# Kernel optimization log

Hardware: AMD Instinct MI355X
Metric: run time of the kernel (lower is better)

Reference implementation:

```python
import jax, jax.numpy as jnp
import numpy as np

N, IN, HID, OUT = 8192, 512, 256, 128

def setup_inputs() -> dict:
    key = jax.random.key(0)
    k1, k2, k3, k4 = jax.random.split(key, 4)
    adj = jax.random.uniform(k1, (N, N), dtype=jnp.float32)
    feature = jax.random.normal(k2, (N, IN), dtype=jnp.float32)
    W1 = jax.random.normal(k3, (IN, HID), dtype=jnp.float32) * (1.0 / np.sqrt(IN))
    b1 = jnp.zeros((HID,), dtype=jnp.float32)
    W2 = jax.random.normal(k4, (HID, OUT), dtype=jnp.float32) * (1.0 / np.sqrt(HID))
    b2 = jnp.zeros((OUT,), dtype=jnp.float32)
    return {"adj": adj, "feature": feature, "W1": W1, "b1": b1, "W2": W2, "b2": b2}

def reference(adj, feature, W1, b1, W2, b2):
    # GCN encoder: layer1 (relu) then layer2 (linear output)
    h = jax.nn.relu(adj @ (feature @ W1) + b1)   # [N, HID]
    h = adj @ (h @ W2) + b2                      # [N, OUT]
    # InnerProductDecoder: sigmoid(flatten(h @ h.T))
    logits = h @ h.T                             # [N, N]
    h_noise = jax.nn.sigmoid(logits.reshape(-1)) # [N*N]
    return (h_noise, h)
```

## Files before the change

### kernel.cpp

```cpp
#include <hip/hip_runtime.h>


typedef __bf16 bf16x8_t __attribute__((ext_vector_type(8)));
typedef __bf16 bf16x4_t __attribute__((ext_vector_type(4)));
typedef float  f32x4_t  __attribute__((ext_vector_type(4)));

#define MFMA_BF16(a, b, c) __builtin_amdgcn_mfma_f32_16x16x32_bf16((a), (b), (c), 0, 0, 0)

__device__ __forceinline__ bf16x8_t cvt8(float4 u, float4 v) {
    bf16x8_t o;
    o[0] = (__bf16)u.x; o[1] = (__bf16)u.y; o[2] = (__bf16)u.z; o[3] = (__bf16)u.w;
    o[4] = (__bf16)v.x; o[5] = (__bf16)v.y; o[6] = (__bf16)v.z; o[7] = (__bf16)v.w;
    return o;
}

__device__ __forceinline__ void gload_lds16(const void* g, void* l) {
    __builtin_amdgcn_global_load_lds(
        (const __attribute__((address_space(1))) unsigned int*)g,
        (__attribute__((address_space(3))) unsigned int*)l, 16, 0, 0);
}

__global__ __launch_bounds__(256) void cast_adj(
    const float* __restrict__ adj, __bf16* __restrict__ ab)
{
    const size_t j = (size_t)blockIdx.x * 256 + threadIdx.x;
    const float4* p = (const float4*)adj + j * 2;
    float4 u = p[0], v = p[1];
    *(bf16x8_t*)(ab + j * 8) = cvt8(u, v);
}

__global__ __launch_bounds__(256) void cast_all(
    const float* __restrict__ feat, const float* __restrict__ W1,
    const float* __restrict__ W2, __bf16* __restrict__ fb,
    __bf16* __restrict__ w1t, __bf16* __restrict__ w2t)
{
    const int j = blockIdx.x * 256 + threadIdx.x;
    if (j < 524288) {
        const float4* p = (const float4*)feat + (size_t)j * 2;
        float4 u = p[0], v = p[1];
        *(bf16x8_t*)(fb + (size_t)j * 8) = cvt8(u, v);
    } else if (j < 524288 + 131072) {
        int t = j - 524288;
        int k = t >> 8, n = t & 255;
        w1t[n * 512 + k] = (__bf16)W1[t];
    } else if (j < 524288 + 131072 + 32768) {
        int t = j - 655360;
        int k = t >> 7, n = t & 127;
        w2t[n * 256 + k] = (__bf16)W2[t];
    }
}

template<int MT, int WC>
__global__ __launch_bounds__(256, 2) void gemm_bt_cbf16(
    const __bf16* __restrict__ X, const __bf16* __restrict__ Yb,
    __bf16* __restrict__ C, int K, int N)
{
    constexpr int WR = 4 / WC;
    constexpr int BM = WR * MT * 16;
    constexpr int BN = WC * 64;
    const int mblk = blockIdx.x, nblk = blockIdx.y;
    const int w = threadIdx.x >> 6, lane = threadIdx.x & 63;
    const int wr = w / WC, wc = w % WC;
    const int q = lane >> 4, l16 = lane & 15;
    const int mbase = mblk * BM + wr * (MT * 16);
    const int nbase = nblk * BN + wc * 64;

    f32x4_t acc[MT][4];
    const f32x4_t z = {0.f, 0.f, 0.f, 0.f};
#pragma unroll
    for (int i = 0; i < MT; i++)
#pragma unroll
        for (int jj = 0; jj < 4; jj++) acc[i][jj] = z;

    const __bf16* Xr[MT];
    const __bf16* Yr[4];
#pragma unroll
    for (int i = 0; i < MT; i++) Xr[i] = X + (size_t)(mbase + i * 16 + l16) * K + q * 8;
#pragma unroll
    for (int jj = 0; jj < 4; jj++) Yr[jj] = Yb + (size_t)(nbase + jj * 16 + l16) * K + q * 8;

    for (int k = 0; k < K; k += 32) {
        bf16x8_t a[MT], b[4];
#pragma unroll
        for (int i = 0; i < MT; i++) a[i] = *(const bf16x8_t*)(Xr[i] + k);
#pragma unroll
        for (int jj = 0; jj < 4; jj++) b[jj] = *(const bf16x8_t*)(Yr[jj] + k);
#pragma unroll
        for (int i = 0; i < MT; i++)
#pragma unroll
            for (int jj = 0; jj < 4; jj++) acc[i][jj] = MFMA_BF16(a[i], b[jj], acc[i][jj]);
    }

#pragma unroll
    for (int i = 0; i < MT; i++)
#pragma unroll
        for (int jj = 0; jj < 4; jj++) {
            const int row0 = mbase + i * 16 + q * 4;
            const int col = nbase + jj * 16 + l16;
#pragma unroll
            for (int r = 0; r < 4; r++)
                C[(size_t)(row0 + r) * N + col] = (__bf16)acc[i][jj][r];
        }
}

template<int NN>
__global__ __launch_bounds__(256, 2) void gemm_adj_m97(
    const __bf16* __restrict__ A, const __bf16* __restrict__ Y,
    float* __restrict__ P, int kchunk)
{
    __shared__ __bf16 As[2][8192];
    __shared__ __bf16 Bs[2][8192];

    const int mblk = blockIdx.x;
    const int nblk = blockIdx.y;
    const int ks   = blockIdx.z;
    const int w = threadIdx.x >> 6, lane = threadIdx.x & 63;
    const int wr = w >> 1, wc = w & 1;
    const int q = lane >> 4, l16 = lane & 15;
    const int kbase = ks * kchunk;
    const int ntiles = kchunk >> 6;

    const int srow = lane >> 3;
    const int gdst = lane & 7;
    const __bf16* gA[4];
    const __bf16* gB[4];
    int lofs[4];
#pragma unroll
    for (int j = 0; j < 4; j++) {
        const int row = (w * 4 + j) * 8 + srow;
        const int gs = gdst ^ (row & 7);
        gA[j] = A + (size_t)(mblk * 128 + row) * 8192 + kbase + gs * 8;
        gB[j] = Y + (size_t)(nblk * 128 + row) * 8192 + kbase + gs * 8;
        lofs[j] = row * 64 + gdst * 8;
    }

    f32x4_t acc[4][4];
    const f32x4_t z = {0.f, 0.f, 0.f, 0.f};
#pragma unroll
    for (int i = 0; i < 4; i++)
#pragma unroll
        for (int jj = 0; jj < 4; jj++) acc[i][jj] = z;

#pragma unroll
    for (int j = 0; j < 4; j++) {
        gload_lds16(gA[j], &As[0][0] + lofs[j]);
        gload_lds16(gB[j], &Bs[0][0] + lofs[j]);
    }

    int buf = 0;
    for (int kt = 0; kt < ntiles; kt++) {
        __syncthreads();

        if (kt + 1 < ntiles) {
            const int koff = (kt + 1) << 6;
#pragma unroll
            for (int j = 0; j < 4; j++) {
                gload_lds16(gA[j] + koff, &As[buf ^ 1][0] + lofs[j]);
                gload_lds16(gB[j] + koff, &Bs[buf ^ 1][0] + lofs[j]);
            }
        }

        const __bf16* __restrict__ LA = &As[buf][0];
        const __bf16* __restrict__ LB = &Bs[buf][0];
#pragma unroll
        for (int s = 0; s < 2; s++) {
            bf16x8_t a[4], b[4];
#pragma unroll
            for (int i = 0; i < 4; i++) {
                const int r = wr * 64 + i * 16 + l16;
                const int g = ((s * 4 + q) ^ (r & 7)) * 8;
                a[i] = *(const bf16x8_t*)(LA + r * 64 + g);
            }
#pragma unroll
            for (int jj = 0; jj < 4; jj++) {
                const int r = wc * 64 + jj * 16 + l16;
                const int g = ((s * 4 + q) ^ (r & 7)) * 8;
                b[jj] = *(const bf16x8_t*)(LB + r * 64 + g);
            }
#pragma unroll
            for (int i = 0; i < 4; i++)
#pragma unroll
                for (int jj = 0; jj < 4; jj++)
                    acc[i][jj] = MFMA_BF16(a[i], b[jj], acc[i][jj]);
        }
        buf ^= 1;
    }

#pragma unroll
    for (int i = 0; i < 4; i++)
#pragma unroll
        for (int jj = 0; jj < 4; jj++) {
            const int row0 = mblk * 128 + wr * 64 + i * 16 + q * 4;
            const int col = nblk * 128 + wc * 64 + jj * 16 + l16;
            float* pp = P + ((size_t)ks * 8192 + row0) * NN + col;
#pragma unroll
            for (int r = 0; r < 4; r++) pp[(size_t)r * NN] = acc[i][jj][r];
        }
}

__global__ __launch_bounds__(256) void epi_relu_bias(
    const float* __restrict__ P, const float* __restrict__ bias,
    __bf16* __restrict__ H)
{
    const size_t SL = (size_t)8192 * 256;
    const size_t idx = ((size_t)blockIdx.x * 256 + threadIdx.x) * 4;
    float4 s;
    s.x = s.y = s.z = s.w = 0.f;
#pragma unroll
    for (int k = 0; k < 4; k++) {
        float4 t = *(const float4*)(P + k * SL + idx);
        s.x += t.x; s.y += t.y; s.z += t.z; s.w += t.w;
    }
    const int col = (int)(idx & 255);
    float4 bb = *(const float4*)(bias + col);
    bf16x4_t o;
    o[0] = (__bf16)fmaxf(s.x + bb.x, 0.f);
    o[1] = (__bf16)fmaxf(s.y + bb.y, 0.f);
    o[2] = (__bf16)fmaxf(s.z + bb.z, 0.f);
    o[3] = (__bf16)fmaxf(s.w + bb.w, 0.f);
    *(bf16x4_t*)(H + idx) = o;
}

__global__ __launch_bounds__(256) void epi_bias_out(
    const float* __restrict__ P, const float* __restrict__ bias,
    float* __restrict__ Hout, __bf16* __restrict__ Hbf)
{
    const size_t SL = (size_t)8192 * 128;
    const size_t idx = ((size_t)blockIdx.x * 256 + threadIdx.x) * 4;
    float4 s;
    s.x = s.y = s.z = s.w = 0.f;
#pragma unroll
    for (int k = 0; k < 8; k++) {
        float4 t = *(const float4*)(P + k * SL + idx);
        s.x += t.x; s.y += t.y; s.z += t.z; s.w += t.w;
    }
    const int col = (int)(idx & 127);
    float4 bb = *(const float4*)(bias + col);
    float4 o;
    o.x = s.x + bb.x; o.y = s.y + bb.y; o.z = s.z + bb.z; o.w = s.w + bb.w;
    *(float4*)(Hout + idx) = o;
    bf16x4_t ob;
    ob[0] = (__bf16)o.x; ob[1] = (__bf16)o.y; ob[2] = (__bf16)o.z; ob[3] = (__bf16)o.w;
    *(bf16x4_t*)(Hbf + idx) = ob;
}

__global__ __launch_bounds__(256, 2) void gemm_sig(
    const __bf16* __restrict__ H, float* __restrict__ out)
{
    const int mblk = blockIdx.x, nblk = blockIdx.y;
    const int w = threadIdx.x >> 6, lane = threadIdx.x & 63;
    const int wr = w >> 1, wc = w & 1;
    const int q = lane >> 4, l16 = lane & 15;
    const int mbase = mblk * 128 + wr * 64;
    const int nbase = nblk * 128 + wc * 64;

    f32x4_t acc[4][4];
    const f32x4_t z = {0.f, 0.f, 0.f, 0.f};
#pragma unroll
    for (int i = 0; i < 4; i++)
#pragma unroll
        for (int jj = 0; jj < 4; jj++) acc[i][jj] = z;

#pragma unroll
    for (int k = 0; k < 128; k += 32) {
        bf16x8_t a[4], b[4];
#pragma unroll
        for (int i = 0; i < 4; i++)
            a[i] = *(const bf16x8_t*)(H + (size_t)(mbase + i * 16 + l16) * 128 + k + q * 8);
#pragma unroll
        for (int jj = 0; jj < 4; jj++)
            b[jj] = *(const bf16x8_t*)(H + (size_t)(nbase + jj * 16 + l16) * 128 + k + q * 8);
#pragma unroll
        for (int i = 0; i < 4; i++)
#pragma unroll
            for (int jj = 0; jj < 4; jj++) acc[i][jj] = MFMA_BF16(a[i], b[jj], acc[i][jj]);
    }

#pragma unroll
    for (int i = 0; i < 4; i++)
#pragma unroll
        for (int jj = 0; jj < 4; jj++) {
            const int row0 = mbase + i * 16 + q * 4;
            const int col = nbase + jj * 16 + l16;
#pragma unroll
            for (int r = 0; r < 4; r++) {
                float x = acc[i][jj][r];
                out[(size_t)(row0 + r) * 8192 + col] = 1.0f / (1.0f + __expf(-x));
            }
        }
}

extern "C" void kernel_launch(void* const* d_in, const int* in_sizes, int n_in,
                              void* d_out, int out_size, void* d_ws, size_t ws_size,
                              hipStream_t stream)
{
    const float* adj  = (const float*)d_in[0];
    const float* feat = (const float*)d_in[1];
    const float* W1   = (const float*)d_in[2];
    const float* b1   = (const float*)d_in[3];
    const float* W2   = (const float*)d_in[4];
    const float* b2   = (const float*)d_in[5];
    float* out = (float*)d_out;

    char* p = (char*)d_ws;
    __bf16* adjbf  = (__bf16*)p; p += (size_t)8192 * 8192 * 2;
    __bf16* featbf = (__bf16*)p; p += (size_t)8192 * 512 * 2;
    __bf16* W1T    = (__bf16*)p; p += (size_t)256 * 512 * 2;
    __bf16* W2T    = (__bf16*)p; p += (size_t)128 * 256 * 2;
    __bf16* t1T    = (__bf16*)p; p += (size_t)256 * 8192 * 2;
    __bf16* h1     = (__bf16*)p; p += (size_t)8192 * 256 * 2;
    __bf16* t2T    = (__bf16*)p; p += (size_t)128 * 8192 * 2;
    __bf16* hbf    = (__bf16*)p; p += (size_t)8192 * 128 * 2;
    float* part    = (float*)p;

    cast_adj<<<32768, 256, 0, stream>>>(adj, adjbf);
    cast_all<<<2688, 256, 0, stream>>>(feat, W1, W2, featbf, W1T, W2T);
    gemm_bt_cbf16<2, 2><<<dim3(4, 64), 256, 0, stream>>>(W1T, featbf, t1T, 512, 8192);
    gemm_adj_m97<256><<<dim3(64, 2, 4), 256, 0, stream>>>(adjbf, t1T, part, 2048);
    epi_relu_bias<<<2048, 256, 0, stream>>>(part, b1, h1);
    gemm_bt_cbf16<1, 2><<<dim3(4, 64), 256, 0, stream>>>(W2T, h1, t2T, 256, 8192);
    gemm_adj_m97<128><<<dim3(64, 1, 8), 256, 0, stream>>>(adjbf, t2T, part, 1024);
    epi_bias_out<<<1024, 256, 0, stream>>>(part, b2, out + (size_t)8192 * 8192, hbf);
    gemm_sig<<<dim3(64, 64), 256, 0, stream>>>(hbf, out);
}
```

Baseline: 650.3 us.

## Load B operand directly to registers, fuse cast kernels, double split-K

New measurement: 714.7 us. 1.1x slower.

```diff
diff --git a/kernel.cpp b/kernel.cpp
--- a/kernel.cpp
+++ b/kernel.cpp
@@ -20,21 +20,21 @@
         (__attribute__((address_space(3))) unsigned int*)l, 16, 0, 0);
 }
 
-__global__ __launch_bounds__(256) void cast_adj(
-    const float* __restrict__ adj, __bf16* __restrict__ ab)
-{
-    const size_t j = (size_t)blockIdx.x * 256 + threadIdx.x;
-    const float4* p = (const float4*)adj + j * 2;
-    float4 u = p[0], v = p[1];
-    *(bf16x8_t*)(ab + j * 8) = cvt8(u, v);
-}
-
-__global__ __launch_bounds__(256) void cast_all(
-    const float* __restrict__ feat, const float* __restrict__ W1,
-    const float* __restrict__ W2, __bf16* __restrict__ fb,
+__global__ __launch_bounds__(256) void cast_fused(
+    const float* __restrict__ adj, const float* __restrict__ feat,
+    const float* __restrict__ W1, const float* __restrict__ W2,
+    __bf16* __restrict__ ab, __bf16* __restrict__ fb,
     __bf16* __restrict__ w1t, __bf16* __restrict__ w2t)
 {
-    const int j = blockIdx.x * 256 + threadIdx.x;
+    const int b = blockIdx.x;
+    if (b < 32768) {
+        const size_t j = (size_t)b * 256 + threadIdx.x;
+        const float4* p = (const float4*)adj + j * 2;
+        float4 u = p[0], v = p[1];
+        *(bf16x8_t*)(ab + j * 8) = cvt8(u, v);
+        return;
+    }
+    const int j = (b - 32768) * 256 + threadIdx.x;
     if (j < 524288) {
         const float4* p = (const float4*)feat + (size_t)j * 2;
         float4 u = p[0], v = p[1];
@@ -104,12 +104,11 @@
 }
 
 template<int NN>
-__global__ __launch_bounds__(256, 2) void gemm_adj_m97(
+__global__ __launch_bounds__(256, 3) void gemm_adj_r7(
     const __bf16* __restrict__ A, const __bf16* __restrict__ Y,
     float* __restrict__ P, int kchunk)
 {
     __shared__ __bf16 As[2][8192];
-    __shared__ __bf16 Bs[2][8192];
 
     const int mblk = blockIdx.x;
     const int nblk = blockIdx.y;
@@ -123,16 +122,19 @@
     const int srow = lane >> 3;
     const int gdst = lane & 7;
     const __bf16* gA[4];
-    const __bf16* gB[4];
     int lofs[4];
 #pragma unroll
     for (int j = 0; j < 4; j++) {
         const int row = (w * 4 + j) * 8 + srow;
         const int gs = gdst ^ (row & 7);
         gA[j] = A + (size_t)(mblk * 128 + row) * 8192 + kbase + gs * 8;
-        gB[j] = Y + (size_t)(nblk * 128 + row) * 8192 + kbase + gs * 8;
         lofs[j] = row * 64 + gdst * 8;
     }
+
+    const __bf16* Yr[4];
+#pragma unroll
+    for (int jj = 0; jj < 4; jj++)
+        Yr[jj] = Y + (size_t)(nblk * 128 + wc * 64 + jj * 16 + l16) * 8192 + q * 8;
 
     f32x4_t acc[4][4];
     const f32x4_t z = {0.f, 0.f, 0.f, 0.f};
@@ -142,29 +144,32 @@
         for (int jj = 0; jj < 4; jj++) acc[i][jj] = z;
 
 #pragma unroll
-    for (int j = 0; j < 4; j++) {
-        gload_lds16(gA[j], &As[0][0] + lofs[j]);
-        gload_lds16(gB[j], &Bs[0][0] + lofs[j]);
-    }
+    for (int j = 0; j < 4; j++) gload_lds16(gA[j], &As[0][0] + lofs[j]);
 
     int buf = 0;
     for (int kt = 0; kt < ntiles; kt++) {
+        const int kk = kbase + (kt << 6);
+
         __syncthreads();
+
+        bf16x8_t breg[2][4];
+#pragma unroll
+        for (int s = 0; s < 2; s++)
+#pragma unroll
+            for (int jj = 0; jj < 4; jj++)
+                breg[s][jj] = *(const bf16x8_t*)(Yr[jj] + kk + s * 32);
 
         if (kt + 1 < ntiles) {
             const int koff = (kt + 1) << 6;
 #pragma unroll
-            for (int j = 0; j < 4; j++) {
+            for (int j = 0; j < 4; j++)
                 gload_lds16(gA[j] + koff, &As[buf ^ 1][0] + lofs[j]);
-                gload_lds16(gB[j] + koff, &Bs[buf ^ 1][0] + lofs[j]);
-            }
         }
 
         const __bf16* __restrict__ LA = &As[buf][0];
-        const __bf16* __restrict__ LB = &Bs[buf][0];
 #pragma unroll
         for (int s = 0; s < 2; s++) {
-            bf16x8_t a[4], b[4];
+            bf16x8_t a[4];
 #pragma unroll
             for (int i = 0; i < 4; i++) {
                 const int r = wr * 64 + i * 16 + l16;
@@ -172,16 +177,10 @@
                 a[i] = *(const bf16x8_t*)(LA + r * 64 + g);
             }
 #pragma unroll
-            for (int jj = 0; jj < 4; jj++) {
-                const int r = wc * 64 + jj * 16 + l16;
-                const int g = ((s * 4 + q) ^ (r & 7)) * 8;
-                b[jj] = *(const bf16x8_t*)(LB + r * 64 + g);
-            }
-#pragma unroll
             for (int i = 0; i < 4; i++)
 #pragma unroll
                 for (int jj = 0; jj < 4; jj++)
-                    acc[i][jj] = MFMA_BF16(a[i], b[jj], acc[i][jj]);
+                    acc[i][jj] = MFMA_BF16(a[i], breg[s][jj], acc[i][jj]);
         }
         buf ^= 1;
     }
@@ -207,7 +206,7 @@
     float4 s;
     s.x = s.y = s.z = s.w = 0.f;
 #pragma unroll
-    for (int k = 0; k < 4; k++) {
+    for (int k = 0; k < 8; k++) {
         float4 t = *(const float4*)(P + k * SL + idx);
         s.x += t.x; s.y += t.y; s.z += t.z; s.w += t.w;
     }
@@ -230,7 +229,7 @@
     float4 s;
     s.x = s.y = s.z = s.w = 0.f;
 #pragma unroll
-    for (int k = 0; k < 8; k++) {
+    for (int k = 0; k < 16; k++) {
         float4 t = *(const float4*)(P + k * SL + idx);
         s.x += t.x; s.y += t.y; s.z += t.z; s.w += t.w;
     }
@@ -313,13 +312,12 @@
     __bf16* hbf    = (__bf16*)p; p += (size_t)8192 * 128 * 2;
     float* part    = (float*)p;
 
-    cast_adj<<<32768, 256, 0, stream>>>(adj, adjbf);
-    cast_all<<<2688, 256, 0, stream>>>(feat, W1, W2, featbf, W1T, W2T);
-    gemm_bt_cbf16<2, 2><<<dim3(4, 64), 256, 0, stream>>>(W1T, featbf, t1T, 512, 8192);
-    gemm_adj_m97<256><<<dim3(64, 2, 4), 256, 0, stream>>>(adjbf, t1T, part, 2048);
+    cast_fused<<<35456, 256, 0, stream>>>(adj, feat, W1, W2, adjbf, featbf, W1T, W2T);
+    gemm_bt_cbf16<1, 2><<<dim3(8, 64), 256, 0, stream>>>(W1T, featbf, t1T, 512, 8192);
+    gemm_adj_r7<256><<<dim3(64, 2, 8), 256, 0, stream>>>(adjbf, t1T, part, 1024);
     epi_relu_bias<<<2048, 256, 0, stream>>>(part, b1, h1);
     gemm_bt_cbf16<1, 2><<<dim3(4, 64), 256, 0, stream>>>(W2T, h1, t2T, 256, 8192);
-    gemm_adj_m97<128><<<dim3(64, 1, 8), 256, 0, stream>>>(adjbf, t2T, part, 1024);
+    gemm_adj_r7<128><<<dim3(64, 1, 16), 256, 0, stream>>>(adjbf, t2T, part, 512);
     epi_bias_out<<<1024, 256, 0, stream>>>(part, b2, out + (size_t)8192 * 8192, hbf);
     gemm_sig<<<dim3(64, 64), 256, 0, stream>>>(hbf, out);
 }
```
